# Optimization experiments

Hardware: AMD Instinct MI355X
Metric: run time of the kernel (lower is better)

## Reference

```python
import jax, jax.numpy as jnp
import numpy as np

N_HEADS = 16
D_HEAD = 64
D_MODEL = 1024
CHUNK = 64
SCALE = 1.0 / np.sqrt(D_HEAD).astype(np.float32)


def binarize(x):
    # {-1,+1} with straight-through gradient (identity in bwd)
    return x + jax.lax.stop_gradient(jnp.where(x >= 0, 1.0, -1.0).astype(x.dtype) - x)


def setup_inputs() -> dict:
    key = jax.random.key(0)
    k1, k2, k3 = jax.random.split(key, 3)
    B, T, D = 2, 4096, D_MODEL
    x = jax.random.normal(k1, (B, T, D), dtype=jnp.float32)
    w_qkv = jax.random.normal(k2, (3 * D, D), dtype=jnp.float32) * (1.0 / np.sqrt(D))
    w_o = jax.random.normal(k3, (D, D), dtype=jnp.float32) * (1.0 / np.sqrt(D))
    return {"x": x, "w_qkv": w_qkv, "w_o": w_o}


def reference(x, w_qkv, w_o):
    B, T, D = x.shape
    H, d, C = N_HEADS, D_HEAD, CHUNK
    qkv = (x @ w_qkv.T).reshape(B, T, 3, H, d)
    q, k, v = qkv[:, :, 0], qkv[:, :, 1], qkv[:, :, 2]
    # -> (B, H, T, d)
    q = jnp.transpose(q, (0, 2, 1, 3)) * jnp.asarray(SCALE, x.dtype)
    k = binarize(jnp.transpose(k, (0, 2, 1, 3)))
    v = binarize(jnp.transpose(v, (0, 2, 1, 3)))

    assert T % C == 0  # T=4096 divisible by chunk=64 (pad branch not exercised)
    Nc = T // C
    qc = q.reshape(B, H, Nc, C, d)
    kc = k.reshape(B, H, Nc, C, d)
    vc = v.reshape(B, H, Nc, C, d)

    causal_mask = jnp.tril(jnp.ones((C, C), dtype=x.dtype))
    # intra-chunk: (B,H,N,C,C) scores, causal-masked, times values
    intra_scores = jnp.einsum('bhnid,bhnjd->bhnij', qc, kc) * causal_mask
    intra = jnp.einsum('bhnij,bhnjd->bhnid', intra_scores, vc)
    # per-chunk KV outer-product state: (B,H,N,d,d)
    chunk_kv = jnp.einsum('bhntk,bhntv->bhnkv', kc, vc)
    prefix = jnp.cumsum(chunk_kv, axis=2) - chunk_kv  # exclusive prefix
    cross = jnp.einsum('bhnck,bhnkv->bhncv', qc, prefix)
    output = (intra + cross).reshape(B, H, T, d)

    final_state = prefix[:, :, -1] + chunk_kv[:, :, -1]
    out = jnp.transpose(output, (0, 2, 1, 3)).reshape(B, T, D)
    return out @ w_o.T, final_state
```

## Files before the change

kernel.cpp:

```cpp
#include <hip/hip_runtime.h>

typedef __bf16 bf16;
typedef __bf16 bf16x8 __attribute__((ext_vector_type(8)));
typedef _Float16 f16;
typedef _Float16 f16x8 __attribute__((ext_vector_type(8)));
typedef float f32x4 __attribute__((ext_vector_type(4)));
typedef short s16x8 __attribute__((ext_vector_type(8)));

#define SCALE 0.125f
#define AP 72
#define CT 128

__device__ __forceinline__ void async_ld16(const void* g, void* l) {
  __builtin_amdgcn_global_load_lds((const __attribute__((address_space(1))) void*)g,
                                   (__attribute__((address_space(3))) void*)l, 16, 0, 0);
}

__global__ __launch_bounds__(256) void k_convert(
    const float* __restrict__ x, const float* __restrict__ wqkv, const float* __restrict__ wo,
    bf16* __restrict__ xsplit, bf16* __restrict__ wsplit, f16* __restrict__ wo16)
{
  const int N1 = 2097152, N2 = 786432, N3 = 262144;
  const int i = blockIdx.x * 256 + threadIdx.x;
  if (i < N1) {
    f32x4 v = ((const f32x4*)x)[i];
    int e = i * 4, m = e >> 10, c = e & 1023;
    bf16 hi[4], lo[4];
#pragma unroll
    for (int u = 0; u < 4; ++u) { hi[u] = (bf16)v[u]; lo[u] = (bf16)(v[u] - (float)hi[u]); }
    *(ulong1*)&xsplit[(size_t)m * 2048 + c] = *(ulong1*)hi;
    *(ulong1*)&xsplit[(size_t)m * 2048 + 1024 + c] = *(ulong1*)lo;
  } else if (i < N1 + N2) {
    int j = i - N1;
    f32x4 v = ((const f32x4*)wqkv)[j];
    int e = j * 4, n = e >> 10, c = e & 1023;
    bf16 hi[4], lo[4];
#pragma unroll
    for (int u = 0; u < 4; ++u) { hi[u] = (bf16)v[u]; lo[u] = (bf16)(v[u] - (float)hi[u]); }
    *(ulong1*)&wsplit[(size_t)n * 2048 + c] = *(ulong1*)hi;
    *(ulong1*)&wsplit[(size_t)n * 2048 + 1024 + c] = *(ulong1*)lo;
  } else if (i < N1 + N2 + N3) {
    int j = i - N1 - N2;
    f32x4 v = ((const f32x4*)wo)[j];
    f16 h[4];
#pragma unroll
    for (int u = 0; u < 4; ++u) h[u] = (f16)v[u];
    *(ulong1*)&wo16[(size_t)j * 4] = *(ulong1*)h;
  }
}

__global__ __launch_bounds__(256) void k_gemm_qkv(
    const bf16* __restrict__ A, const bf16* __restrict__ B,
    bf16* __restrict__ Qws, bf16* __restrict__ Kws, bf16* __restrict__ Vws)
{
  __shared__ char smem[32768];
  const int tid = threadIdx.x;
  const int wave = tid >> 6, lane = tid & 63;
  const int quad = lane >> 4, l16 = lane & 15;
  const int l = blockIdx.x;
  int mb, nbr;
  if (l < 1024) { mb = l & 63; nbr = 8 + (l >> 6); }
  else          { const int q = l - 1024; mb = q & 63; nbr = q >> 6; }
  const int n0 = nbr * 128;
  const int m0 = mb * 128;
  const int wm = (wave >> 1) << 6, wn = (wave & 1) << 6;
  const int region = n0 >> 10;
  f32x4 acc[4][4] = {};

  if (region == 0) {
    bf16* As = (bf16*)smem;
    bf16* Bs = As + 128 * 64;
    const int r8 = lane >> 3, c8 = lane & 7;
    const int sw = l16 & 7;
    const int srcoff = (c8 ^ r8) * 8;
    for (int k0 = 0; k0 < 1024; k0 += 64) {
      __syncthreads();
#pragma unroll
      for (int it = 0; it < 4; ++it) {
        const int row = wave * 32 + it * 8 + r8;
        async_ld16(A + (size_t)(m0 + row) * 2048 + k0 + srcoff, As + row * 64 + c8 * 8);
        async_ld16(B + (size_t)(n0 + row) * 2048 + k0 + srcoff, Bs + row * 64 + c8 * 8);
      }
      __syncthreads();
#pragma unroll
      for (int ks = 0; ks < 64; ks += 32) {
        bf16x8 af[4], bg[4];
#pragma unroll
        for (int mi = 0; mi < 4; ++mi)
          af[mi] = *(const bf16x8*)&As[(wm + mi * 16 + l16) * 64 + ((((ks >> 3) + quad) ^ sw) << 3)];
#pragma unroll
        for (int ni = 0; ni < 4; ++ni)
          bg[ni] = *(const bf16x8*)&Bs[(wn + ni * 16 + l16) * 64 + ((((ks >> 3) + quad) ^ sw) << 3)];
#pragma unroll
        for (int mi = 0; mi < 4; ++mi)
#pragma unroll
          for (int ni = 0; ni < 4; ++ni)
            acc[mi][ni] = __builtin_amdgcn_mfma_f32_16x16x32_bf16(af[mi], bg[ni], acc[mi][ni], 0, 0, 0);
      }
    }
  } else {
    bf16* Ah = (bf16*)smem;
    bf16* Al = Ah + 128 * 32;
    bf16* Bh = Al + 128 * 32;
    bf16* Bl = Bh + 128 * 32;
    const int rr0 = tid >> 2;
    const int sl = tid & 3;
    const int rsw = quad ^ ((l16 >> 1) & 3);
    for (int k0 = 0; k0 < 1024; k0 += 32) {
      __syncthreads();
#pragma unroll
      for (int rr = 0; rr < 2; ++rr) {
        const int row = rr * 64 + rr0;
        const int soff = ((sl ^ ((row >> 1) & 3)) << 3);
        const bf16* arow = A + (size_t)(m0 + row) * 2048 + k0 + soff;
        const bf16* brow = B + (size_t)(n0 + row) * 2048 + k0 + soff;
        async_ld16(arow,        Ah + row * 32 + sl * 8);
        async_ld16(arow + 1024, Al + row * 32 + sl * 8);
        async_ld16(brow,        Bh + row * 32 + sl * 8);
        async_ld16(brow + 1024, Bl + row * 32 + sl * 8);
      }
      __syncthreads();
#pragma unroll
      for (int cb = 0; cb < 3; ++cb) {
        const bf16* Asrc = (cb == 1) ? Al : Ah;
        const bf16* Bsrc = (cb == 2) ? Bl : Bh;
        bf16x8 af[4], bg[4];
#pragma unroll
        for (int mi = 0; mi < 4; ++mi)
          af[mi] = *(const bf16x8*)&Asrc[(wm + mi * 16 + l16) * 32 + (rsw << 3)];
#pragma unroll
        for (int ni = 0; ni < 4; ++ni)
          bg[ni] = *(const bf16x8*)&Bsrc[(wn + ni * 16 + l16) * 32 + (rsw << 3)];
#pragma unroll
        for (int mi = 0; mi < 4; ++mi)
#pragma unroll
          for (int ni = 0; ni < 4; ++ni)
            acc[mi][ni] = __builtin_amdgcn_mfma_f32_16x16x32_bf16(af[mi], bg[ni], acc[mi][ni], 0, 0, 0);
      }
    }
  }

  bf16* Ct = (bf16*)smem;
  __syncthreads();
#pragma unroll
  for (int mi = 0; mi < 4; ++mi) {
    const int ml = wm + mi * 16 + quad * 4;
#pragma unroll
    for (int ni = 0; ni < 4; ++ni) {
      const int nl = wn + ni * 16 + l16;
#pragma unroll
      for (int r = 0; r < 4; ++r) {
        const float v = acc[mi][ni][r];
        bf16 o;
        if (region == 0) o = (bf16)(v * SCALE);
        else             o = (bf16)((v >= 0.f) ? 1.f : -1.f);
        Ct[(ml + r) * CT + nl] = o;
      }
    }
  }
  __syncthreads();
  {
    const int row = tid >> 1, half = tid & 1;
    const int nn = (n0 & 1023) + half * 64;
    const int h = nn >> 6;
    const int b = m0 >> 12, t = (m0 & 4095) + row;
    bf16* base = (region == 0) ? Qws : (region == 1) ? Kws : Vws;
    bf16* dst = base + ((size_t)(b * 16 + h) * 4096 + t) * 64;
    const bf16* src = &Ct[row * CT + half * 64];
#pragma unroll
    for (int u = 0; u < 8; ++u)
      *(bf16x8*)(dst + u * 8) = *(const bf16x8*)(src + u * 8);
  }
}

__global__ __launch_bounds__(256) void k_ckv(
    const bf16* __restrict__ Kws, const bf16* __restrict__ Vws, short* __restrict__ ckv)
{
  __shared__ bf16 Kt[64 * AP];
  __shared__ bf16 Vt[64 * AP];
  const int tid = threadIdx.x;
  const int nchunk = blockIdx.x & 63, bh = blockIdx.x >> 6;
  const size_t tbase = ((size_t)bh * 4096 + (size_t)nchunk * 64) * 64;
  const int row = tid >> 2, c0 = (tid & 3) << 4;
  {
    const bf16x8* gk = (const bf16x8*)(Kws + tbase + row * 64 + c0);
    const bf16x8* gv = (const bf16x8*)(Vws + tbase + row * 64 + c0);
    bf16x8 k0 = gk[0], k1 = gk[1], v0 = gv[0], v1 = gv[1];
#pragma unroll
    for (int u = 0; u < 8; ++u) {
      Kt[(c0 + u) * AP + row] = k0[u];
      Kt[(c0 + 8 + u) * AP + row] = k1[u];
      Vt[(c0 + u) * AP + row] = v0[u];
      Vt[(c0 + 8 + u) * AP + row] = v1[u];
    }
  }
  __syncthreads();
  const int wave = tid >> 6, lane = tid & 63;
  const int quad = lane >> 4, l16 = lane & 15;
  const int ti = wave;
  bf16x8 ka[2];
#pragma unroll
  for (int kk = 0; kk < 2; ++kk)
    ka[kk] = *(const bf16x8*)&Kt[(ti * 16 + l16) * AP + kk * 32 + quad * 8];
  short* dst = ckv + ((size_t)bh * 64 + nchunk) * 4096;
#pragma unroll
  for (int td = 0; td < 4; ++td) {
    f32x4 acc = {};
#pragma unroll
    for (int kk = 0; kk < 2; ++kk) {
      const bf16x8 vb = *(const bf16x8*)&Vt[(td * 16 + l16) * AP + kk * 32 + quad * 8];
      acc = __builtin_amdgcn_mfma_f32_16x16x32_bf16(ka[kk], vb, acc, 0, 0, 0);
    }
#pragma unroll
    for (int r = 0; r < 4; ++r)
      dst[(ti * 16 + quad * 4 + r) * 64 + td * 16 + l16] = (short)acc[r];
  }
}

__global__ __launch_bounds__(256) void k_scan(short* __restrict__ ckv, float* __restrict__ fin)
{
  const int idx2 = blockIdx.x * 256 + threadIdx.x;
  short* p = ckv + ((size_t)(idx2 >> 11)) * 262144 + (size_t)(idx2 & 2047) * 2;
  int r0 = 0, r1 = 0;
#pragma unroll
  for (int n = 0; n < 64; ++n) {
    unsigned int w = *(unsigned int*)(p + (size_t)n * 4096);
    const short a = (short)(w & 0xffff);
    const short bb = (short)(w >> 16);
    *(unsigned int*)(p + (size_t)n * 4096) =
        ((unsigned int)(unsigned short)(short)r0) | (((unsigned int)(unsigned short)(short)r1) << 16);
    r0 += a; r1 += bb;
  }
  float2 f; f.x = (float)r0; f.y = (float)r1;
  *(float2*)(fin + ((size_t)(idx2 >> 11)) * 4096 + (size_t)(idx2 & 2047) * 2) = f;
}

__global__ __launch_bounds__(256) void k_attn(
    const bf16* __restrict__ Qws, const bf16* __restrict__ Kws, const bf16* __restrict__ Vws,
    const short* __restrict__ pref, f16* __restrict__ attn)
{
  __shared__ bf16 Ks[64 * 64];
  __shared__ bf16 Vt[64 * AP];
  __shared__ bf16 Ph[64 * AP];
  __shared__ bf16 Pl[64 * AP];
  __shared__ bf16 Ss[64 * AP];
  const int tid = threadIdx.x;
  const int nchunk = blockIdx.x & 63, bh = blockIdx.x >> 6;
  const int b = bh >> 4, h = bh & 15;
  const size_t tbase = ((size_t)bh * 4096 + (size_t)nchunk * 64) * 64;

  {
    const int c8 = tid & 7, r0 = tid >> 3;
#pragma unroll
    for (int it = 0; it < 2; ++it) {
      const int row = it * 32 + r0;
      async_ld16(Kws + tbase + row * 64 + ((c8 ^ (row & 7)) << 3), Ks + row * 64 + (c8 << 3));
    }
  }
  const int wave = tid >> 6, lane = tid & 63;
  const int quad = lane >> 4, l16 = lane & 15;
  const int ti = wave;
  bf16x8 qa[2];
#pragma unroll
  for (int kk = 0; kk < 2; ++kk)
    qa[kk] = *(const bf16x8*)(Qws + tbase + (ti * 16 + l16) * 64 + kk * 32 + quad * 8);
  {
    const int row = tid >> 2, c0 = (tid & 3) << 4;
    const bf16x8* gv = (const bf16x8*)(Vws + tbase + row * 64 + c0);
    bf16x8 v0 = gv[0], v1 = gv[1];
#pragma unroll
    for (int u = 0; u < 8; ++u) {
      Vt[(c0 + u) * AP + row] = v0[u];
      Vt[(c0 + 8 + u) * AP + row] = v1[u];
    }
    const short* gp = pref + ((size_t)bh * 64 + nchunk) * 4096 + row * 64 + c0;
    s16x8 p0 = *(const s16x8*)(gp);
    s16x8 p1 = *(const s16x8*)(gp + 8);
#pragma unroll
    for (int u = 0; u < 8; ++u) {
      {
        const float p = (float)p0[u];
        const bf16 hi = (bf16)p;
        Ph[(c0 + u) * AP + row] = hi;
        Pl[(c0 + u) * AP + row] = (bf16)(p - (float)hi);
      }
      {
        const float p = (float)p1[u];
        const bf16 hi = (bf16)p;
        Ph[(c0 + 8 + u) * AP + row] = hi;
        Pl[(c0 + 8 + u) * AP + row] = (bf16)(p - (float)hi);
      }
    }
  }
  __syncthreads();

  const int sw = l16 & 7;
  f32x4 sacc[4] = {};
#pragma unroll
  for (int tj = 0; tj < 4; ++tj)
#pragma unroll
    for (int kk = 0; kk < 2; ++kk) {
      const bf16x8 kb = *(const bf16x8*)&Ks[(tj * 16 + l16) * 64 + (((kk * 4 + quad) ^ sw) << 3)];
      sacc[tj] = __builtin_amdgcn_mfma_f32_16x16x32_bf16(qa[kk], kb, sacc[tj], 0, 0, 0);
    }
#pragma unroll
  for (int tj = 0; tj < 4; ++tj)
#pragma unroll
    for (int r = 0; r < 4; ++r) {
      const int i = ti * 16 + quad * 4 + r;
      const int jj = tj * 16 + l16;
      Ss[i * AP + jj] = (bf16)((jj <= i) ? sacc[tj][r] : 0.f);
    }
  __syncthreads();

  bf16x8 sa[2];
#pragma unroll
  for (int kk = 0; kk < 2; ++kk)
    sa[kk] = *(const bf16x8*)&Ss[(ti * 16 + l16) * AP + kk * 32 + quad * 8];
  f32x4 oacc[4] = {};
#pragma unroll
  for (int td = 0; td < 4; ++td) {
#pragma unroll
    for (int kk = 0; kk < 2; ++kk) {
      const bf16x8 vb = *(const bf16x8*)&Vt[(td * 16 + l16) * AP + kk * 32 + quad * 8];
      oacc[td] = __builtin_amdgcn_mfma_f32_16x16x32_bf16(sa[kk], vb, oacc[td], 0, 0, 0);
    }
#pragma unroll
    for (int kk = 0; kk < 2; ++kk) {
      const bf16x8 pb = *(const bf16x8*)&Ph[(td * 16 + l16) * AP + kk * 32 + quad * 8];
      oacc[td] = __builtin_amdgcn_mfma_f32_16x16x32_bf16(qa[kk], pb, oacc[td], 0, 0, 0);
      const bf16x8 pb2 = *(const bf16x8*)&Pl[(td * 16 + l16) * AP + kk * 32 + quad * 8];
      oacc[td] = __builtin_amdgcn_mfma_f32_16x16x32_bf16(qa[kk], pb2, oacc[td], 0, 0, 0);
    }
  }
  __syncthreads();
  f16* Os = (f16*)Ss;
#pragma unroll
  for (int td = 0; td < 4; ++td)
#pragma unroll
    for (int r = 0; r < 4; ++r) {
      const int i = ti * 16 + quad * 4 + r;
      const int dd = td * 16 + l16;
      Os[i * AP + dd] = (f16)oacc[td][r];
    }
  __syncthreads();
  {
    const int i2 = tid >> 2, q4 = tid & 3;
    const int t = nchunk * 64 + i2;
    f16* dst = attn + ((size_t)(b * 4096 + t)) * 1024 + h * 64 + q4 * 16;
    const f16* src = &Os[i2 * AP + q4 * 16];
    *(f16x8*)(dst) = *(const f16x8*)(src);
    *(f16x8*)(dst + 8) = *(const f16x8*)(src + 8);
  }
}

__global__ __launch_bounds__(256) void k_gemm_out(
    const f16* __restrict__ A, const f16* __restrict__ B, float* __restrict__ out)
{
  __shared__ f16 As[128 * 64];
  __shared__ f16 Bs[128 * 64];
  const int tid = threadIdx.x;
  const int wave = tid >> 6, lane = tid & 63;
  const int quad = lane >> 4, l16 = lane & 15;
  const int bidl = blockIdx.x;
  const int m0 = (bidl & 63) << 7;
  const int n0 = (bidl >> 6) << 7;
  const int wm = (wave >> 1) << 6, wn = (wave & 1) << 6;
  const int r8 = lane >> 3, c8 = lane & 7;
  const int sw = l16 & 7;
  const int srcoff = (c8 ^ r8) * 8;
  f32x4 acc[4][4] = {};

  for (int k0 = 0; k0 < 1024; k0 += 64) {
    __syncthreads();
#pragma unroll
    for (int it = 0; it < 4; ++it) {
      const int row = wave * 32 + it * 8 + r8;
      async_ld16(A + (size_t)(m0 + row) * 1024 + k0 + srcoff, As + row * 64 + c8 * 8);
      async_ld16(B + (size_t)(n0 + row) * 1024 + k0 + srcoff, Bs + row * 64 + c8 * 8);
    }
    __syncthreads();
#pragma unroll
    for (int ks = 0; ks < 64; ks += 32) {
      f16x8 af[4], bg[4];
#pragma unroll
      for (int mi = 0; mi < 4; ++mi)
        af[mi] = *(const f16x8*)&As[(wm + mi * 16 + l16) * 64 + ((((ks >> 3) + quad) ^ sw) << 3)];
#pragma unroll
      for (int ni = 0; ni < 4; ++ni)
        bg[ni] = *(const f16x8*)&Bs[(wn + ni * 16 + l16) * 64 + ((((ks >> 3) + quad) ^ sw) << 3)];
#pragma unroll
      for (int mi = 0; mi < 4; ++mi)
#pragma unroll
        for (int ni = 0; ni < 4; ++ni)
          acc[mi][ni] = __builtin_amdgcn_mfma_f32_16x16x32_f16(af[mi], bg[ni], acc[mi][ni], 0, 0, 0);
    }
  }
#pragma unroll
  for (int mi = 0; mi < 4; ++mi)
#pragma unroll
    for (int ni = 0; ni < 4; ++ni)
#pragma unroll
      for (int r = 0; r < 4; ++r) {
        const int m = m0 + wm + mi * 16 + quad * 4 + r;
        const int n = n0 + wn + ni * 16 + l16;
        out[(size_t)m * 1024 + n] = acc[mi][ni][r];
      }
}

extern "C" void kernel_launch(void* const* d_in, const int* in_sizes, int n_in,
                              void* d_out, int out_size, void* d_ws, size_t ws_size,
                              hipStream_t stream)
{
  const float* x = (const float*)d_in[0];
  const float* wqkv = (const float*)d_in[1];
  const float* wo = (const float*)d_in[2];
  float* out = (float*)d_out;
  char* ws = (char*)d_ws;

  bf16* xsplit = (bf16*)(ws);
  bf16* wsplit = (bf16*)(ws + 33554432);
  f16*  wo16   = (f16*)(ws + 46137344);
  bf16* Qws    = (bf16*)(ws + 48234496);
  bf16* Kws    = (bf16*)(ws + 65011712);
  bf16* Vws    = (bf16*)(ws + 81788928);
  short* ckv   = (short*)(ws + 98566144);
  f16*  attn   = (f16*)(ws + 132120576);
  float* fin   = out + 8388608;

  k_convert<<<12288, 256, 0, stream>>>(x, wqkv, wo, xsplit, wsplit, wo16);
  k_gemm_qkv<<<1536, 256, 0, stream>>>(xsplit, wsplit, Qws, Kws, Vws);
  k_ckv<<<2048, 256, 0, stream>>>(Kws, Vws, ckv);
  k_scan<<<256, 256, 0, stream>>>(ckv, fin);
  k_attn<<<2048, 256, 0, stream>>>(Qws, Kws, Vws, ckv, attn);
  k_gemm_out<<<512, 256, 0, stream>>>(attn, wo16, out);
}
```

Measured before the change: 271.8 us.

## Precompute transposed hi/lo bf16 prefix state in scan and async-load it in attention

The chunk KV kernel now writes the state transposed (V-major). The scan converts the prefix sums to bf16 hi/lo pairs and writes them to global memory in a swizzled layout, replacing the in-place short write-back. The attention kernel then loads these prefix tiles directly into LDS with async global-to-LDS copies instead of loading shorts, converting them and doing scattered transposed LDS stores. This trades double the prefix bytes written by the scan (two bf16 arrays reusing the xsplit workspace) for less conversion and LDS scatter work in attention. The final state is written with a transposed strided store.

```diff
diff --git a/kernel.cpp b/kernel.cpp
--- a/kernel.cpp
+++ b/kernel.cpp
@@ -198,18 +198,18 @@
   const int wave = tid >> 6, lane = tid & 63;
   const int quad = lane >> 4, l16 = lane & 15;
   const int ti = wave;
-  bf16x8 ka[2];
+  bf16x8 va[2];
 #pragma unroll
   for (int kk = 0; kk < 2; ++kk)
-    ka[kk] = *(const bf16x8*)&Kt[(ti * 16 + l16) * AP + kk * 32 + quad * 8];
+    va[kk] = *(const bf16x8*)&Vt[(ti * 16 + l16) * AP + kk * 32 + quad * 8];
   short* dst = ckv + ((size_t)bh * 64 + nchunk) * 4096;
 #pragma unroll
   for (int td = 0; td < 4; ++td) {
     f32x4 acc = {};
 #pragma unroll
     for (int kk = 0; kk < 2; ++kk) {
-      const bf16x8 vb = *(const bf16x8*)&Vt[(td * 16 + l16) * AP + kk * 32 + quad * 8];
-      acc = __builtin_amdgcn_mfma_f32_16x16x32_bf16(ka[kk], vb, acc, 0, 0, 0);
+      const bf16x8 kb = *(const bf16x8*)&Kt[(td * 16 + l16) * AP + kk * 32 + quad * 8];
+      acc = __builtin_amdgcn_mfma_f32_16x16x32_bf16(va[kk], kb, acc, 0, 0, 0);
     }
 #pragma unroll
     for (int r = 0; r < 4; ++r)
@@ -217,32 +217,44 @@
   }
 }
 
-__global__ __launch_bounds__(256) void k_scan(short* __restrict__ ckv, float* __restrict__ fin)
+__global__ __launch_bounds__(256) void k_scan(
+    const short* __restrict__ ckv, bf16* __restrict__ Ph, bf16* __restrict__ Pl,
+    float* __restrict__ fin)
 {
   const int idx2 = blockIdx.x * 256 + threadIdx.x;
-  short* p = ckv + ((size_t)(idx2 >> 11)) * 262144 + (size_t)(idx2 & 2047) * 2;
+  const int bh = idx2 >> 11, p = idx2 & 2047;
+  const int dd = p >> 5, ii0 = (p & 31) << 1;
+  const int colp = ((((ii0 >> 3) ^ (dd & 7)) << 3) | (ii0 & 7));
+  const short* src = ckv + (size_t)bh * 262144 + dd * 64 + ii0;
+  bf16* ph = Ph + (size_t)bh * 262144 + dd * 64 + colp;
+  bf16* pl = Pl + (size_t)bh * 262144 + dd * 64 + colp;
   int r0 = 0, r1 = 0;
 #pragma unroll
   for (int n = 0; n < 64; ++n) {
-    unsigned int w = *(unsigned int*)(p + (size_t)n * 4096);
+    const unsigned int w = *(const unsigned int*)(src + (size_t)n * 4096);
     const short a = (short)(w & 0xffff);
     const short bb = (short)(w >> 16);
-    *(unsigned int*)(p + (size_t)n * 4096) =
-        ((unsigned int)(unsigned short)(short)r0) | (((unsigned int)(unsigned short)(short)r1) << 16);
+    const float f0 = (float)r0, f1 = (float)r1;
+    const bf16 h0 = (bf16)f0, h1 = (bf16)f1;
+    bf16 hv[2] = {h0, h1};
+    bf16 lv[2] = {(bf16)(f0 - (float)h0), (bf16)(f1 - (float)h1)};
+    *(unsigned int*)(ph + (size_t)n * 4096) = *(unsigned int*)hv;
+    *(unsigned int*)(pl + (size_t)n * 4096) = *(unsigned int*)lv;
     r0 += a; r1 += bb;
   }
-  float2 f; f.x = (float)r0; f.y = (float)r1;
-  *(float2*)(fin + ((size_t)(idx2 >> 11)) * 4096 + (size_t)(idx2 & 2047) * 2) = f;
+  float* fb = fin + (size_t)bh * 4096;
+  fb[ii0 * 64 + dd] = (float)r0;
+  fb[(ii0 + 1) * 64 + dd] = (float)r1;
 }
 
 __global__ __launch_bounds__(256) void k_attn(
     const bf16* __restrict__ Qws, const bf16* __restrict__ Kws, const bf16* __restrict__ Vws,
-    const short* __restrict__ pref, f16* __restrict__ attn)
+    const bf16* __restrict__ Ph, const bf16* __restrict__ Pl, f16* __restrict__ attn)
 {
   __shared__ bf16 Ks[64 * 64];
   __shared__ bf16 Vt[64 * AP];
-  __shared__ bf16 Ph[64 * AP];
-  __shared__ bf16 Pl[64 * AP];
+  __shared__ bf16 Phs[64 * 64];
+  __shared__ bf16 Pls[64 * 64];
   __shared__ bf16 Ss[64 * AP];
   const int tid = threadIdx.x;
   const int nchunk = blockIdx.x & 63, bh = blockIdx.x >> 6;
@@ -251,10 +263,14 @@
 
   {
     const int c8 = tid & 7, r0 = tid >> 3;
+    const bf16* gph = Ph + ((size_t)bh * 64 + nchunk) * 4096;
+    const bf16* gpl = Pl + ((size_t)bh * 64 + nchunk) * 4096;
 #pragma unroll
     for (int it = 0; it < 2; ++it) {
       const int row = it * 32 + r0;
       async_ld16(Kws + tbase + row * 64 + ((c8 ^ (row & 7)) << 3), Ks + row * 64 + (c8 << 3));
+      async_ld16(gph + row * 64 + (c8 << 3), Phs + row * 64 + (c8 << 3));
+      async_ld16(gpl + row * 64 + (c8 << 3), Pls + row * 64 + (c8 << 3));
     }
   }
   const int wave = tid >> 6, lane = tid & 63;
@@ -273,24 +289,6 @@
       Vt[(c0 + u) * AP + row] = v0[u];
       Vt[(c0 + 8 + u) * AP + row] = v1[u];
     }
-    const short* gp = pref + ((size_t)bh * 64 + nchunk) * 4096 + row * 64 + c0;
-    s16x8 p0 = *(const s16x8*)(gp);
-    s16x8 p1 = *(const s16x8*)(gp + 8);
-#pragma unroll
-    for (int u = 0; u < 8; ++u) {
-      {
-        const float p = (float)p0[u];
-        const bf16 hi = (bf16)p;
-        Ph[(c0 + u) * AP + row] = hi;
-        Pl[(c0 + u) * AP + row] = (bf16)(p - (float)hi);
-      }
-      {
-        const float p = (float)p1[u];
-        const bf16 hi = (bf16)p;
-        Ph[(c0 + 8 + u) * AP + row] = hi;
-        Pl[(c0 + 8 + u) * AP + row] = (bf16)(p - (float)hi);
-      }
-    }
   }
   __syncthreads();
 
@@ -320,16 +318,17 @@
   f32x4 oacc[4] = {};
 #pragma unroll
   for (int td = 0; td < 4; ++td) {
+    const int prow = td * 16 + l16;
 #pragma unroll
     for (int kk = 0; kk < 2; ++kk) {
-      const bf16x8 vb = *(const bf16x8*)&Vt[(td * 16 + l16) * AP + kk * 32 + quad * 8];
+      const bf16x8 vb = *(const bf16x8*)&Vt[prow * AP + kk * 32 + quad * 8];
       oacc[td] = __builtin_amdgcn_mfma_f32_16x16x32_bf16(sa[kk], vb, oacc[td], 0, 0, 0);
     }
 #pragma unroll
     for (int kk = 0; kk < 2; ++kk) {
-      const bf16x8 pb = *(const bf16x8*)&Ph[(td * 16 + l16) * AP + kk * 32 + quad * 8];
+      const bf16x8 pb = *(const bf16x8*)&Phs[prow * 64 + (((kk * 4 + quad) ^ sw) << 3)];
       oacc[td] = __builtin_amdgcn_mfma_f32_16x16x32_bf16(qa[kk], pb, oacc[td], 0, 0, 0);
-      const bf16x8 pb2 = *(const bf16x8*)&Pl[(td * 16 + l16) * AP + kk * 32 + quad * 8];
+      const bf16x8 pb2 = *(const bf16x8*)&Pls[prow * 64 + (((kk * 4 + quad) ^ sw) << 3)];
       oacc[td] = __builtin_amdgcn_mfma_f32_16x16x32_bf16(qa[kk], pb2, oacc[td], 0, 0, 0);
     }
   }
@@ -426,12 +425,14 @@
   bf16* Vws    = (bf16*)(ws + 81788928);
   short* ckv   = (short*)(ws + 98566144);
   f16*  attn   = (f16*)(ws + 132120576);
+  bf16* Ph     = (bf16*)(ws);
+  bf16* Pl     = (bf16*)(ws + 16777216);
   float* fin   = out + 8388608;
 
   k_convert<<<12288, 256, 0, stream>>>(x, wqkv, wo, xsplit, wsplit, wo16);
   k_gemm_qkv<<<1536, 256, 0, stream>>>(xsplit, wsplit, Qws, Kws, Vws);
   k_ckv<<<2048, 256, 0, stream>>>(Kws, Vws, ckv);
-  k_scan<<<256, 256, 0, stream>>>(ckv, fin);
-  k_attn<<<2048, 256, 0, stream>>>(Qws, Kws, Vws, ckv, attn);
+  k_scan<<<256, 256, 0, stream>>>(ckv, Ph, Pl, fin);
+  k_attn<<<2048, 256, 0, stream>>>(Qws, Kws, Vws, Ph, Pl, attn);
   k_gemm_out<<<512, 256, 0, stream>>>(attn, wo16, out);
 }
```

Measured after the change: 282.1 us. 3.8% more time.
